# Performance work log

Hardware: AMD Instinct MI355X
Metric: run time of the kernel (lower is better)

## Reference

```python
import jax, jax.numpy as jnp
import numpy as np


def setup_inputs() -> dict:
    key = jax.random.key(0)
    k1, k2, k3, k4 = jax.random.split(key, 4)
    H = W = 1024
    B = 16
    image = jax.random.normal(k1, (1, H, W), dtype=jnp.float32)
    x = jax.random.normal(k2, (B, 1, H, W), dtype=jnp.float32)
    # Conv2d(1, 9, 3) parameters, torch layout: weight (out=9, in=1, 3, 3), bias (9,)
    fan_in = 1 * 3 * 3
    bound = 1.0 / np.sqrt(fan_in)
    W_KL = jax.random.uniform(k3, (9, 1, 3, 3), jnp.float32, -bound, bound)
    b_KL = jax.random.uniform(k4, (9,), jnp.float32, -bound, bound)
    return {"image": image, "x": x, "W_KL": W_KL, "b_KL": b_KL}


def reference(image, x, W_KL, b_KL):
    # K = Conv2d(image): (1,H,W) -> (9,H,W), 'same' padding
    K = jax.lax.conv_general_dilated(
        image[None], W_KL, window_strides=(1, 1), padding='SAME',
        dimension_numbers=('NCHW', 'OIHW', 'NCHW'))[0] + b_KL[:, None, None]
    H, W = image.shape[1], image.shape[2]
    # permute (9,H,W) -> (H,W,9) -> unflatten to per-pixel 3x3 kernels (H,W,3,3)
    K = jnp.transpose(K, (1, 2, 0)).reshape(H, W, 3, 3)
    # Apply spatially-varying 3x3 kernel: y[b,c,h,w] = sum_{a,d} K[h,w,a,d] * x_pad[b,c,h+a,w+d]
    x_pad = jnp.pad(x, ((0, 0), (0, 0), (1, 1), (1, 1)))
    y = jnp.zeros_like(x)
    for a in range(3):
        for d in range(3):
            y = y + K[:, :, a, d] * x_pad[:, :, a:a + H, d:d + W]
    return y
```

## Files before the change

### kernel.cpp

```cpp
#include <hip/hip_runtime.h>

#define IH 1024
#define IW 1024
#define NB 16
#define NB2 8

typedef float v4f __attribute__((ext_vector_type(4)));

#define VMWAIT(n) asm volatile("s_waitcnt vmcnt(" #n ")" ::: "memory")
#define SCHEDB()  __builtin_amdgcn_sched_barrier(0)

__device__ __forceinline__ void glds16(const float* g, float* l) {
    __builtin_amdgcn_global_load_lds(
        (const __attribute__((address_space(1))) void*)g,
        (__attribute__((address_space(3))) void*)l, 16, 0, 0);
}

struct RawWin { v4f mv[3]; float fl[3]; float fr[3]; };

__device__ __forceinline__ void issue_win(const float* __restrict__ plane,
                                          int h, int w0, RawWin& rw) {
#pragma unroll
    for (int a = 0; a < 3; ++a) {
        const int hh = h + a - 1;
        const int hc = (hh < 0) ? 0 : (hh >= IH ? IH - 1 : hh);
        const float* rowp = plane + (size_t)hc * IW;
        rw.fl[a] = rowp[w0 > 0 ? w0 - 1 : 0];
        rw.mv[a] = *(const v4f*)(rowp + w0);
        rw.fr[a] = rowp[w0 + 4 < IW ? w0 + 4 : IW - 1];
    }
}

__device__ __forceinline__ void fin_win_img(const RawWin& rw, int h, int w0,
                                            float win[3][6]) {
#pragma unroll
    for (int a = 0; a < 3; ++a) {
        const int hh = h + a - 1;
        const bool rowok = (hh >= 0) & (hh < IH);
        win[a][0] = (rowok && w0 > 0)      ? rw.fl[a]   : 0.f;
        win[a][1] = rowok ? rw.mv[a].x : 0.f;
        win[a][2] = rowok ? rw.mv[a].y : 0.f;
        win[a][3] = rowok ? rw.mv[a].z : 0.f;
        win[a][4] = rowok ? rw.mv[a].w : 0.f;
        win[a][5] = (rowok && w0 + 4 < IW) ? rw.fr[a]   : 0.f;
    }
}

__global__ __launch_bounds__(256, 4) void fused_d3(
    const float* __restrict__ image,
    const float* __restrict__ x,
    const float* __restrict__ Wk,
    const float* __restrict__ bk,
    float* __restrict__ out)
{
    __shared__ float lds[3][6][256];

    const int tx = threadIdx.x;
    const int wv = threadIdx.y;

    const int hwid  = blockIdx.x;
    const int xcd   = hwid & 7;
    const int chunk = hwid >> 3;
    const int bz    = chunk & 1;
    const int bx    = (chunk >> 1) & 3;
    const int g     = xcd * 32 + (chunk >> 3);
    const int c0    = bx * 256;
    const int h0    = g * 4;
    const int h     = h0 + wv;
    const int lc    = tx * 4;
    const int w0    = c0 + lc;
    const int b0    = bz * NB2;

    const size_t plane = (size_t)IH * IW;

    int zv; asm("v_mov_b32 %0, 0" : "=v"(zv));

    auto stage = [&](int gb, int buf) {
        const float* xb = x + (size_t)gb * plane;
        int gr = h0 - 1 + wv; gr = gr < 0 ? 0 : gr;
        glds16(xb + (size_t)gr * IW + c0 + tx * 4, &lds[buf][wv][0]);
        if (wv < 2) {
            int g2 = h0 + 3 + wv; g2 = g2 > IH - 1 ? IH - 1 : g2;
            glds16(xb + (size_t)g2 * IW + c0 + tx * 4, &lds[buf][wv + 4][0]);
        }
    };
    auto halo = [&](int gb, float* HL, float* HR) {
        const float* xb = x + (size_t)gb * plane;
        const int cl = (c0 > 0) ? c0 - 1 : 0;
        const int cr = (c0 + 256 < IW) ? c0 + 256 : IW - 1;
#pragma unroll
        for (int a = 0; a < 3; ++a) {
            int gr = h + a - 1; gr = gr < 0 ? 0 : (gr > IH - 1 ? IH - 1 : gr);
            const float* rp = xb + (size_t)gr * IW;
            HL[a] = rp[cl + zv];
            HR[a] = rp[cr + zv];
        }
    };

    RawWin rimg;
    issue_win(image, h, w0, rimg);
    SCHEDB();
    float hl[3][3], hr[3][3];
    stage(b0, 0);                 SCHEDB();
    halo(b0, hl[0], hr[0]);       SCHEDB();
    stage(b0 + 1, 1);             SCHEDB();
    halo(b0 + 1, hl[1], hr[1]);   SCHEDB();

    float wkk[81];
#pragma unroll
    for (int i = 0; i < 81; ++i) wkk[i] = Wk[i];
    float bb[9];
#pragma unroll
    for (int c = 0; c < 9; ++c) bb[c] = bk[c];

    float p[3][6];
    fin_win_img(rimg, h, w0, p);
    float Kv[4][9];
#pragma unroll
    for (int j = 0; j < 4; ++j)
#pragma unroll
        for (int c = 0; c < 9; ++c) {
            float acc = bb[c];
#pragma unroll
            for (int a = 0; a < 3; ++a)
#pragma unroll
                for (int d = 0; d < 3; ++d)
                    acc = fmaf(wkk[c * 9 + a * 3 + d], p[a][j + d], acc);
            Kv[j][c] = acc;
        }
    {
        const bool top = (h == 0);
        const bool bot = (h == IH - 1);
#pragma unroll
        for (int j = 0; j < 4; ++j)
#pragma unroll
            for (int d = 0; d < 3; ++d) {
                Kv[j][d]     = top ? 0.f : Kv[j][d];
                Kv[j][6 + d] = bot ? 0.f : Kv[j][6 + d];
            }
    }

    if (wv < 2) { VMWAIT(14); } else { VMWAIT(13); }
    SCHEDB();
    __builtin_amdgcn_s_barrier();
    SCHEDB();

    v4f yprev;
    float* obp = out + (size_t)h * IW + w0;
    const int ll = (tx > 0)  ? lc - 4 : 0;
    const int lr = (tx < 63) ? lc + 4 : 252;

#pragma unroll
    for (int b = 0; b < NB2; ++b) {
        const int gb = b0 + b;
        if (b > 0) {
            __builtin_nontemporal_store(yprev,
                                        (v4f*)(obp + (size_t)(gb - 1) * plane));
            SCHEDB();
        }
        if (b + 2 < NB2) {
            stage(gb + 2, (b + 2) % 3);                      SCHEDB();
            halo(gb + 2, hl[(b + 2) % 3], hr[(b + 2) % 3]);  SCHEDB();
        }
        {
            const float* lb = &lds[b % 3][0][0];
            float win[3][6];
#pragma unroll
            for (int a = 0; a < 3; ++a) {
                const float* rowp = lb + (wv + a) * 256;
                const v4f lv = *(const v4f*)(rowp + ll);
                const v4f mv = *(const v4f*)(rowp + lc);
                const v4f rv = *(const v4f*)(rowp + lr);
                const float le = (tx == 0)  ? hl[b % 3][a] : lv.w;
                const float re = (tx == 63) ? hr[b % 3][a] : rv.x;
                win[a][0] = (w0 > 0)      ? le : 0.f;
                win[a][1] = mv.x; win[a][2] = mv.y;
                win[a][3] = mv.z; win[a][4] = mv.w;
                win[a][5] = (w0 + 4 < IW) ? re : 0.f;
            }
            v4f yy;
#pragma unroll
            for (int j = 0; j < 4; ++j) {
                float acc = 0.f;
#pragma unroll
                for (int a = 0; a < 3; ++a)
#pragma unroll
                    for (int d = 0; d < 3; ++d)
                        acc = fmaf(Kv[j][a * 3 + d], win[a][j + d], acc);
                yy[j] = acc;
            }
            yprev = yy;
        }
        if (b + 1 < NB2) {
            if (b == 0)      { if (wv < 2) { VMWAIT(14); } else { VMWAIT(13); } }
            else if (b == 6) { VMWAIT(7); }
            else             { if (wv < 2) { VMWAIT(15); } else { VMWAIT(14); } }
            SCHEDB();
            __builtin_amdgcn_s_barrier();
            SCHEDB();
        }
    }
    __builtin_nontemporal_store(yprev,
                                (v4f*)(obp + (size_t)(b0 + NB2 - 1) * plane));
}

extern "C" void kernel_launch(void* const* d_in, const int* in_sizes, int n_in,
                              void* d_out, int out_size, void* d_ws, size_t ws_size,
                              hipStream_t stream) {
    const float* image = (const float*)d_in[0];
    const float* x     = (const float*)d_in[1];
    const float* Wk    = (const float*)d_in[2];
    const float* bk    = (const float*)d_in[3];
    float* out = (float*)d_out;

    dim3 block(64, 4);
    dim3 grid(2048);
    fused_d3<<<grid, block, 0, stream>>>(image, x, Wk, bk, out);
}
```

Before: 129.2 us.

## Buffer all batch outputs in registers and store at end with double-buffered LDS

```diff
diff --git a/kernel.cpp b/kernel.cpp
--- a/kernel.cpp
+++ b/kernel.cpp
@@ -46,14 +46,14 @@
     }
 }
 
-__global__ __launch_bounds__(256, 4) void fused_d3(
+__global__ __launch_bounds__(256, 4) void fused_regout(
     const float* __restrict__ image,
     const float* __restrict__ x,
     const float* __restrict__ Wk,
     const float* __restrict__ bk,
     float* __restrict__ out)
 {
-    __shared__ float lds[3][6][256];
+    __shared__ float lds[2][6][256];
 
     const int tx = threadIdx.x;
     const int wv = threadIdx.y;
@@ -100,7 +100,7 @@
     RawWin rimg;
     issue_win(image, h, w0, rimg);
     SCHEDB();
-    float hl[3][3], hr[3][3];
+    float hl[2][3], hr[2][3];
     stage(b0, 0);                 SCHEDB();
     halo(b0, hl[0], hr[0]);       SCHEDB();
     stage(b0 + 1, 1);             SCHEDB();
@@ -145,25 +145,19 @@
     __builtin_amdgcn_s_barrier();
     SCHEDB();
 
-    v4f yprev;
-    float* obp = out + (size_t)h * IW + w0;
+    v4f yacc[NB2];
     const int ll = (tx > 0)  ? lc - 4 : 0;
     const int lr = (tx < 63) ? lc + 4 : 252;
 
 #pragma unroll
     for (int b = 0; b < NB2; ++b) {
         const int gb = b0 + b;
-        if (b > 0) {
-            __builtin_nontemporal_store(yprev,
-                                        (v4f*)(obp + (size_t)(gb - 1) * plane));
-            SCHEDB();
-        }
-        if (b + 2 < NB2) {
-            stage(gb + 2, (b + 2) % 3);                      SCHEDB();
-            halo(gb + 2, hl[(b + 2) % 3], hr[(b + 2) % 3]);  SCHEDB();
+        if (b + 1 < NB2) {
+            stage(gb + 1, (b + 1) & 1);                      SCHEDB();
+            halo(gb + 1, hl[(b + 1) & 1], hr[(b + 1) & 1]);  SCHEDB();
         }
         {
-            const float* lb = &lds[b % 3][0][0];
+            const float* lb = &lds[b & 1][0][0];
             float win[3][6];
 #pragma unroll
             for (int a = 0; a < 3; ++a) {
@@ -171,8 +165,8 @@
                 const v4f lv = *(const v4f*)(rowp + ll);
                 const v4f mv = *(const v4f*)(rowp + lc);
                 const v4f rv = *(const v4f*)(rowp + lr);
-                const float le = (tx == 0)  ? hl[b % 3][a] : lv.w;
-                const float re = (tx == 63) ? hr[b % 3][a] : rv.x;
+                const float le = (tx == 0)  ? hl[b & 1][a] : lv.w;
+                const float re = (tx == 63) ? hr[b & 1][a] : rv.x;
                 win[a][0] = (w0 > 0)      ? le : 0.f;
                 win[a][1] = mv.x; win[a][2] = mv.y;
                 win[a][3] = mv.z; win[a][4] = mv.w;
@@ -189,19 +183,21 @@
                         acc = fmaf(Kv[j][a * 3 + d], win[a][j + d], acc);
                 yy[j] = acc;
             }
-            yprev = yy;
+            yacc[b] = yy;
         }
         if (b + 1 < NB2) {
-            if (b == 0)      { if (wv < 2) { VMWAIT(14); } else { VMWAIT(13); } }
-            else if (b == 6) { VMWAIT(7); }
-            else             { if (wv < 2) { VMWAIT(15); } else { VMWAIT(14); } }
+            VMWAIT(6);
             SCHEDB();
             __builtin_amdgcn_s_barrier();
             SCHEDB();
         }
     }
-    __builtin_nontemporal_store(yprev,
-                                (v4f*)(obp + (size_t)(b0 + NB2 - 1) * plane));
+
+    float* obp = out + (size_t)h * IW + w0;
+#pragma unroll
+    for (int b = 0; b < NB2; ++b)
+        __builtin_nontemporal_store(yacc[b],
+                                    (v4f*)(obp + (size_t)(b0 + b) * plane));
 }
 
 extern "C" void kernel_launch(void* const* d_in, const int* in_sizes, int n_in,
@@ -215,5 +211,5 @@
 
     dim3 block(64, 4);
     dim3 grid(2048);
-    fused_d3<<<grid, block, 0, stream>>>(image, x, Wk, bk, out);
-}
+    fused_regout<<<grid, block, 0, stream>>>(image, x, Wk, bk, out);
+}
```

New measurement: 340.5 us. +163.5%, slower.
